# Performance work log

Hardware: AMD Instinct MI355X
Metric: run time of the kernel (lower is better)

## Reference

```python
import jax, jax.numpy as jnp
import numpy as np

N = 50000
E = 1_600_000
IN_C = 128
HID = 128
HEADS = 4
F_OUT = HID // HEADS  # 32
NEG_SLOPE = 0.2


def _glorot(key, shape):
    fan_in, fan_out = shape[0], shape[-1]
    lim = jnp.sqrt(6.0 / (fan_in + fan_out)).astype(jnp.float32)
    return jax.random.uniform(key, shape, jnp.float32, -lim, lim)


def setup_inputs() -> dict:
    key = jax.random.key(0)
    ks = jax.random.split(key, 12)
    x = jax.random.normal(ks[0], (N, IN_C), jnp.float32)
    edge_index = jax.random.randint(ks[1], (2, E), 0, N, jnp.int32)
    # layer 0 params
    W0 = _glorot(ks[2], (IN_C, HEADS * F_OUT))
    att_src0 = _glorot(ks[3], (HEADS, F_OUT))
    att_dst0 = _glorot(ks[4], (HEADS, F_OUT))
    b0 = jnp.zeros((HEADS * F_OUT,), jnp.float32)
    # layer 1 params
    W1 = _glorot(ks[5], (HID, HEADS * F_OUT))
    att_src1 = _glorot(ks[6], (HEADS, F_OUT))
    att_dst1 = _glorot(ks[7], (HEADS, F_OUT))
    b1 = jnp.zeros((HEADS * F_OUT,), jnp.float32)
    return {"x": x, "edge_index": edge_index,
            "W0": W0, "att_src0": att_src0, "att_dst0": att_dst0, "b0": b0,
            "W1": W1, "att_src1": att_src1, "att_dst1": att_dst1, "b1": b1}


def gat_conv(x, src, dst, W, att_src, att_dst, b):
    n = x.shape[0]
    h = (x @ W).reshape(n, HEADS, F_OUT)              # [N,H,F]
    a_s = jnp.einsum('nhf,hf->nh', h, att_src)        # [N,H]
    a_d = jnp.einsum('nhf,hf->nh', h, att_dst)        # [N,H]
    e = jax.nn.leaky_relu(a_s[src] + a_d[dst], NEG_SLOPE)   # [E,H]
    # segment softmax over destination-node neighborhoods
    e_max = jax.ops.segment_max(e, dst, num_segments=n)     # [N,H]
    e_exp = jnp.exp(e - e_max[dst])                          # [E,H]
    denom = jax.ops.segment_sum(e_exp, dst, num_segments=n)  # [N,H]
    denom = jnp.where(denom > 0, denom, 1.0)
    alpha = e_exp / denom[dst]                               # [E,H]
    msg = alpha[:, :, None] * h[src]                         # [E,H,F]
    out = jax.ops.segment_sum(msg, dst, num_segments=n)      # [N,H,F]
    return out.reshape(n, HEADS * F_OUT) + b


def reference(x, edge_index, W0, att_src0, att_dst0, b0, W1, att_src1, att_dst1, b1):
    src, dst = edge_index[0], edge_index[1]
    h = gat_conv(x, src, dst, W0, att_src0, att_dst0, b0)
    h = jax.nn.relu(h)  # dropout p=0.0 / eval mode -> identity
    out = gat_conv(h, src, dst, W1, att_src1, att_dst1, b1)
    return out
```

## Files before the change

### kernel.cpp

```cpp
#include <hip/hip_runtime.h>
#include <hip/hip_fp16.h>

#define N_NODES 50000
#define N_EDGES 1600000
#define NB 196
#define NBLK 256
#define CHUNK (N_EDGES / NBLK)
#define GEMM_BLOCKS 256

typedef _Float16 half8_t __attribute__((ext_vector_type(8)));
typedef _Float16 half2_t __attribute__((ext_vector_type(2)));
typedef float floatx4 __attribute__((ext_vector_type(4)));

#if defined(__has_builtin)
#  if __has_builtin(__builtin_amdgcn_fdot2)
#    define HAS_FDOT2 1
#  endif
#endif
#ifndef HAS_FDOT2
#  define HAS_FDOT2 0
#endif

__global__ __launch_bounds__(256) void gemm_mfma(const float* __restrict__ Xf,
                                                 const __half* __restrict__ Xh,
                                                 int in_half,
                                                 const float* __restrict__ W,
                                                 const float* __restrict__ att_s,
                                                 const float* __restrict__ att_d,
                                                 __half* __restrict__ H16,
                                                 float* __restrict__ as_out,
                                                 float* __restrict__ ad_out, int nrows,
                                                 const int* __restrict__ hist_dst,
                                                 int* __restrict__ hist_totals) {
    __shared__ __align__(16) char lds[49152];
    int t = threadIdx.x;
    if (hist_totals != nullptr && blockIdx.x >= GEMM_BLOCKS) {
        int* hist = reinterpret_cast<int*>(lds);
        int b = blockIdx.x - GEMM_BLOCKS;
        for (int i = t; i < NB; i += 256) hist[i] = 0;
        __syncthreads();
        int s = b * CHUNK;
        for (int i = t; i < CHUNK; i += 256)
            atomicAdd(&hist[hist_dst[s + i] >> 8], 1);
        __syncthreads();
        for (int i = t; i < NB; i += 256)
            if (hist[i]) atomicAdd(&hist_totals[i], hist[i]);
        return;
    }
    char* Alds = lds;
    char* Wlds = lds + 16384;
    int lane = t & 63, wv_ = t >> 6;
    for (int p = 0; p < 16; ++p) {
        int flat = p * 256 + t;
        int k = flat >> 5;
        int n0 = (flat & 31) * 4;
        float4 wv = reinterpret_cast<const float4*>(W)[flat];
        const float* wf = reinterpret_cast<const float*>(&wv);
        #pragma unroll
        for (int i = 0; i < 4; ++i) {
            int n = n0 + i;
            int byte = (n * 256 + k * 2) ^ ((n & 7) << 4);
            *reinterpret_cast<__half*>(Wlds + byte) = __float2half(wf[i]);
        }
    }
    int col16 = lane & 15;
    float Asv[8], Adv[8];
    #pragma unroll
    for (int nt = 0; nt < 8; ++nt) {
        Asv[nt] = att_s[nt * 16 + col16];
        Adv[nt] = att_d[nt * 16 + col16];
    }
    int ksub = (lane >> 4) * 16;
    int rloc = wv_ * 16 + col16;
    int ntiles = (nrows + 63) / 64;
    for (int tile = blockIdx.x; tile < ntiles; tile += GEMM_BLOCKS) {
        int row0 = tile * 64;
        __syncthreads();
        for (int p = 0; p < 8; ++p) {
            int r = p * 8 + (t >> 5);
            int f4 = t & 31;
            int rr = row0 + r;
            uint2 hv = make_uint2(0, 0);
            if (rr < nrows) {
                if (in_half) {
                    hv = *reinterpret_cast<const uint2*>(Xh + (size_t)rr * 128 + f4 * 4);
                } else {
                    float4 xv = reinterpret_cast<const float4*>(Xf)[(size_t)rr * 32 + f4];
                    __half2* hp = reinterpret_cast<__half2*>(&hv);
                    hp[0] = __floats2half2_rn(xv.x, xv.y);
                    hp[1] = __floats2half2_rn(xv.z, xv.w);
                }
            }
            int byte = (r * 256 + f4 * 8) ^ ((r & 7) << 4);
            *reinterpret_cast<uint2*>(Alds + byte) = hv;
        }
        __syncthreads();
        half8_t afr[4];
        #pragma unroll
        for (int kb = 0; kb < 4; ++kb) {
            int byte = (rloc * 256 + kb * 64 + ksub) ^ ((rloc & 7) << 4);
            afr[kb] = *reinterpret_cast<half8_t*>(Alds + byte);
        }
        floatx4 acc[8];
        #pragma unroll
        for (int nt = 0; nt < 8; ++nt) {
            int n = nt * 16 + col16;
            floatx4 a = {0.f, 0.f, 0.f, 0.f};
            #pragma unroll
            for (int kb = 0; kb < 4; ++kb) {
                int byte = (n * 256 + kb * 64 + ksub) ^ ((n & 7) << 4);
                half8_t bfr = *reinterpret_cast<half8_t*>(Wlds + byte);
                a = __builtin_amdgcn_mfma_f32_16x16x32_f16(afr[kb], bfr, a, 0, 0, 0);
            }
            acc[nt] = a;
        }
        float ps[4][4], pd[4][4];
        #pragma unroll
        for (int reg = 0; reg < 4; ++reg)
            #pragma unroll
            for (int h = 0; h < 4; ++h) {
                ps[reg][h] = acc[2*h][reg] * Asv[2*h] + acc[2*h+1][reg] * Asv[2*h+1];
                pd[reg][h] = acc[2*h][reg] * Adv[2*h] + acc[2*h+1][reg] * Adv[2*h+1];
            }
        #pragma unroll
        for (int m = 1; m <= 8; m <<= 1)
            #pragma unroll
            for (int reg = 0; reg < 4; ++reg)
                #pragma unroll
                for (int h = 0; h < 4; ++h) {
                    ps[reg][h] += __shfl_xor(ps[reg][h], m);
                    pd[reg][h] += __shfl_xor(pd[reg][h], m);
                }
        int rbase = row0 + wv_ * 16 + (lane >> 4) * 4;
        #pragma unroll
        for (int reg = 0; reg < 4; ++reg) {
            int grow = rbase + reg;
            if (grow < nrows) {
                #pragma unroll
                for (int nt = 0; nt < 8; ++nt)
                    H16[(size_t)grow * 128 + nt * 16 + col16] = __float2half(acc[nt][reg]);
                if (col16 == 0) {
                    *reinterpret_cast<float4*>(as_out + (size_t)grow * 4) =
                        make_float4(ps[reg][0], ps[reg][1], ps[reg][2], ps[reg][3]);
                    *reinterpret_cast<float4*>(ad_out + (size_t)grow * 4) =
                        make_float4(pd[reg][0], pd[reg][1], pd[reg][2], pd[reg][3]);
                }
            }
        }
    }
}

__global__ __launch_bounds__(1024) void bucket_scatter(const int* __restrict__ src,
                                                       const int* __restrict__ dst,
                                                       const int* __restrict__ btotal,
                                                       int* __restrict__ bcursor,
                                                       int* __restrict__ bucketed) {
    __shared__ int bexcl[NB];
    __shared__ int hist[NB];
    __shared__ int lstart[NB];
    __shared__ int curL[NB];
    __shared__ int gbase[NB];
    __shared__ int recs[CHUNK];
    __shared__ int srt[CHUNK];
    int t = threadIdx.x, b = blockIdx.x;
    int myTot = 0;
    if (t < NB) { myTot = btotal[t]; bexcl[t] = myTot; }
    for (int i = t; i < NB; i += 1024) hist[i] = 0;
    __syncthreads();
    for (int o = 1; o < NB; o <<= 1) {
        int v = (t < NB && t >= o) ? bexcl[t - o] : 0;
        __syncthreads();
        if (t < NB) bexcl[t] += v;
        __syncthreads();
    }
    if (t < NB) bexcl[t] -= myTot;
    int s0 = b * CHUNK;
    for (int i = t; i < CHUNK; i += 1024) {
        unsigned sv = (unsigned)src[s0 + i], dv = (unsigned)dst[s0 + i];
        recs[i] = (int)((sv << 16) | dv);
        atomicAdd(&hist[dv >> 8], 1);
    }
    __syncthreads();
    int myCnt = (t < NB) ? hist[t] : 0;
    if (t < NB) lstart[t] = myCnt;
    __syncthreads();
    for (int o = 1; o < NB; o <<= 1) {
        int v = (t < NB && t >= o) ? lstart[t - o] : 0;
        __syncthreads();
        if (t < NB) lstart[t] += v;
        __syncthreads();
    }
    if (t < NB) {
        int ex = lstart[t] - myCnt;
        lstart[t] = ex;
        curL[t] = ex;
        gbase[t] = bexcl[t] + atomicAdd(&bcursor[t], myCnt);
    }
    __syncthreads();
    for (int i = t; i < CHUNK; i += 1024) {
        int r = recs[i];
        int bk = (int)(((unsigned)r & 0xFFFFu) >> 8);
        int p = atomicAdd(&curL[bk], 1);
        srt[p] = r;
    }
    __syncthreads();
    for (int p = t; p < CHUNK; p += 1024) {
        int r = srt[p];
        unsigned d = (unsigned)r & 0xFFFFu;
        int bk = (int)(d >> 8);
        int g = gbase[bk] + (p - lstart[bk]);
        bucketed[g] = (int)((((unsigned)r >> 16) << 8) | (d & 255u));
    }
}

__global__ __launch_bounds__(1024) void bucket_sort(const int* __restrict__ bucketed,
                                                    const int* __restrict__ btotal,
                                                    int* __restrict__ sorted_packed,
                                                    int* __restrict__ off) {
    __shared__ int bb[NB];
    __shared__ int cnt[256], scn[256], cur[256];
    int t = threadIdx.x, k = blockIdx.x;
    if (t < NB) bb[t] = btotal[t];
    if (t < 256) cnt[t] = 0;
    __syncthreads();
    for (int o = 1; o < NB; o <<= 1) {
        int v = (t < NB && t >= o) ? bb[t - o] : 0;
        __syncthreads();
        if (t < NB) bb[t] += v;
        __syncthreads();
    }
    int base = (k == 0) ? 0 : bb[k - 1];
    int end  = bb[k];
    int m = end - base;
    for (int i = t; i < m; i += 1024)
        atomicAdd(&cnt[bucketed[base + i] & 255], 1);
    __syncthreads();
    if (t < 256) scn[t] = cnt[t];
    __syncthreads();
    for (int o = 1; o < 256; o <<= 1) {
        int v = (t < 256 && t >= o) ? scn[t - o] : 0;
        __syncthreads();
        if (t < 256) scn[t] += v;
        __syncthreads();
    }
    if (t < 256) {
        int excl = scn[t] - cnt[t];
        cur[t] = base + excl;
        int node = k * 256 + t;
        if (node <= N_NODES) off[node] = base + excl;
    }
    __syncthreads();
    for (int i = t; i < m; i += 1024) {
        int rec = bucketed[base + i];
        int p = atomicAdd(&cur[rec & 255], 1);
        sorted_packed[p] = rec;
    }
}

__global__ __launch_bounds__(256) void gat_aggregate_v3(const __half* __restrict__ H16,
                                                        const int* __restrict__ off,
                                                        const int* __restrict__ packed,
                                                        const float* __restrict__ asb,
                                                        const float* __restrict__ adb,
                                                        const float* __restrict__ bias,
                                                        float* __restrict__ OUTF,
                                                        __half* __restrict__ OUTH,
                                                        int n, int mode) {
    int wid = (blockIdx.x * 256 + threadIdx.x) >> 6;
    int lane = threadIdx.x & 63;
    if (wid >= n) return;
    int s = off[wid], e = off[wid + 1];
    int q = lane >> 4;
    int sub = lane & 15;
    int head4 = (sub >> 2) * 4;
    int sub16 = sub * 16;
    float adv = adb[(size_t)wid * 4 + (sub >> 2)];
    const char* Hc = reinterpret_cast<const char*>(H16);
    const char* Ac = reinterpret_cast<const char*>(asb);
    float acc[8] = {0, 0, 0, 0, 0, 0, 0, 0};
    float den = 0.f;
    if (s < e) {
        int idx[4]; float sc[4];
        #pragma unroll
        for (int u = 0; u < 4; ++u) {
            int ii = s + q + u * 4;
            int jj = ii < e ? ii : s;
            idx[u] = packed[jj] & 0xFFFFFF00;
            sc[u] = *reinterpret_cast<const float*>(Ac + (idx[u] >> 4) + head4);
        }
        for (int i = s; i < e; i += 16) {
            uint4 h0 = *reinterpret_cast<const uint4*>(Hc + idx[0] + sub16);
            uint4 h1 = *reinterpret_cast<const uint4*>(Hc + idx[1] + sub16);
            uint4 h2 = *reinterpret_cast<const uint4*>(Hc + idx[2] + sub16);
            uint4 h3 = *reinterpret_cast<const uint4*>(Hc + idx[3] + sub16);
            float w[4];
            #pragma unroll
            for (int u = 0; u < 4; ++u) {
                float ev = sc[u] + adv; ev = fmaxf(ev, 0.2f * ev);
                w[u] = (i + q + u * 4 < e) ? __expf(ev) : 0.f;
            }
            #pragma unroll
            for (int u = 0; u < 4; ++u) {
                int ii = i + 16 + q + u * 4;
                int jj = ii < e ? ii : s;
                idx[u] = packed[jj] & 0xFFFFFF00;
                sc[u] = *reinterpret_cast<const float*>(Ac + (idx[u] >> 4) + head4);
            }
            den += (w[0] + w[1]) + (w[2] + w[3]);
#if HAS_FDOT2
            half2_t w01 = __builtin_bit_cast(half2_t, __builtin_amdgcn_cvt_pkrtz(w[0], w[1]));
            half2_t w23 = __builtin_bit_cast(half2_t, __builtin_amdgcn_cvt_pkrtz(w[2], w[3]));
            const uint* a0 = reinterpret_cast<const uint*>(&h0);
            const uint* a1 = reinterpret_cast<const uint*>(&h1);
            const uint* a2 = reinterpret_cast<const uint*>(&h2);
            const uint* a3 = reinterpret_cast<const uint*>(&h3);
            #pragma unroll
            for (int j = 0; j < 4; ++j) {
                uint p0 = __builtin_amdgcn_perm(a1[j], a0[j], 0x05040100u);
                uint p1 = __builtin_amdgcn_perm(a1[j], a0[j], 0x07060302u);
                uint r0 = __builtin_amdgcn_perm(a3[j], a2[j], 0x05040100u);
                uint r1 = __builtin_amdgcn_perm(a3[j], a2[j], 0x07060302u);
                acc[2*j]   = __builtin_amdgcn_fdot2(__builtin_bit_cast(half2_t, p0), w01,
                             __builtin_amdgcn_fdot2(__builtin_bit_cast(half2_t, r0), w23, acc[2*j],   false), false);
                acc[2*j+1] = __builtin_amdgcn_fdot2(__builtin_bit_cast(half2_t, p1), w01,
                             __builtin_amdgcn_fdot2(__builtin_bit_cast(half2_t, r1), w23, acc[2*j+1], false), false);
            }
#else
            const __half2* pa = reinterpret_cast<const __half2*>(&h0);
            const __half2* pb = reinterpret_cast<const __half2*>(&h1);
            const __half2* pc = reinterpret_cast<const __half2*>(&h2);
            const __half2* pd_ = reinterpret_cast<const __half2*>(&h3);
            #pragma unroll
            for (int j = 0; j < 4; ++j) {
                float2 fa = __half22float2(pa[j]);
                float2 fb = __half22float2(pb[j]);
                float2 fc = __half22float2(pc[j]);
                float2 fd = __half22float2(pd_[j]);
                acc[2*j]   += w[0] * fa.x + w[1] * fb.x + w[2] * fc.x + w[3] * fd.x;
                acc[2*j+1] += w[0] * fa.y + w[1] * fb.y + w[2] * fc.y + w[3] * fd.y;
            }
#endif
        }
    }
    #pragma unroll
    for (int j = 0; j < 8; ++j) acc[j] += __shfl_xor(acc[j], 16);
    den += __shfl_xor(den, 16);
    #pragma unroll
    for (int j = 0; j < 8; ++j) acc[j] += __shfl_xor(acc[j], 32);
    den += __shfl_xor(den, 32);
    if (q == 0) {
        float inv = den > 0.f ? 1.f / den : 0.f;
        float4 b0 = *reinterpret_cast<const float4*>(bias + sub * 8);
        float4 b1 = *reinterpret_cast<const float4*>(bias + sub * 8 + 4);
        float o[8];
        o[0] = acc[0]*inv + b0.x; o[1] = acc[1]*inv + b0.y;
        o[2] = acc[2]*inv + b0.z; o[3] = acc[3]*inv + b0.w;
        o[4] = acc[4]*inv + b1.x; o[5] = acc[5]*inv + b1.y;
        o[6] = acc[6]*inv + b1.z; o[7] = acc[7]*inv + b1.w;
        if (mode) {
            uint4 u;
            __half2* up = reinterpret_cast<__half2*>(&u);
            #pragma unroll
            for (int j = 0; j < 4; ++j)
                up[j] = __floats2half2_rn(fmaxf(o[2*j], 0.f), fmaxf(o[2*j+1], 0.f));
            *reinterpret_cast<uint4*>(OUTH + (size_t)wid * 128 + sub * 8) = u;
        } else {
            *reinterpret_cast<float4*>(OUTF + (size_t)wid * 128 + sub * 8) =
                make_float4(o[0], o[1], o[2], o[3]);
            *reinterpret_cast<float4*>(OUTF + (size_t)wid * 128 + sub * 8 + 4) =
                make_float4(o[4], o[5], o[6], o[7]);
        }
    }
}

extern "C" void kernel_launch(void* const* d_in, const int* in_sizes, int n_in,
                              void* d_out, int out_size, void* d_ws, size_t ws_size,
                              hipStream_t stream) {
    const float* x        = (const float*)d_in[0];
    const int*   edge     = (const int*)d_in[1];
    const float* W0       = (const float*)d_in[2];
    const float* att_src0 = (const float*)d_in[3];
    const float* att_dst0 = (const float*)d_in[4];
    const float* b0       = (const float*)d_in[5];
    const float* W1       = (const float*)d_in[6];
    const float* att_src1 = (const float*)d_in[7];
    const float* att_dst1 = (const float*)d_in[8];
    const float* b1       = (const float*)d_in[9];
    const int* src = edge;
    const int* dst = edge + N_EDGES;
    float* out = (float*)d_out;

    char* ws = (char*)d_ws;
    size_t o = 0;
    auto alloc = [&](size_t bytes) { char* p = ws + o; o += (bytes + 255) & ~(size_t)255; return p; };
    __half* H16   = (__half*)alloc((size_t)N_NODES * 128 * 2);
    float* asb    = (float*)alloc((size_t)N_NODES * 4 * 4);
    float* adb    = (float*)alloc((size_t)N_NODES * 4 * 4);
    int*   off    = (int*)alloc((size_t)(N_NODES + 1) * 4);
    int*   sorted = (int*)alloc((size_t)N_EDGES * 4);
    size_t mark = o;
    int*   btot2    = (int*)alloc((size_t)2 * NB * 4);
    int*   bucketed = (int*)alloc((size_t)N_EDGES * 4);
    __half* h1_16 = (__half*)(ws + mark);
    int* btotal  = btot2;
    int* bcursor = btot2 + NB;

    int agg_blocks = N_NODES / 4;

    hipMemsetAsync(btot2, 0, (size_t)2 * NB * 4, stream);
    gemm_mfma<<<GEMM_BLOCKS + NBLK, 256, 0, stream>>>(x, (const __half*)nullptr, 0,
                                                      W0, att_src0, att_dst0,
                                                      H16, asb, adb, N_NODES, dst, btotal);
    bucket_scatter<<<NBLK, 1024, 0, stream>>>(src, dst, btotal, bcursor, bucketed);
    bucket_sort<<<NB, 1024, 0, stream>>>(bucketed, btotal, sorted, off);

    gat_aggregate_v3<<<agg_blocks, 256, 0, stream>>>(H16, off, sorted, asb, adb, b0,
                                                     (float*)nullptr, h1_16, N_NODES, 1);

    gemm_mfma<<<GEMM_BLOCKS, 256, 0, stream>>>((const float*)nullptr, h1_16, 1,
                                               W1, att_src1, att_dst1,
                                               H16, asb, adb, N_NODES,
                                               (const int*)nullptr, (int*)nullptr);
    gat_aggregate_v3<<<agg_blocks, 256, 0, stream>>>(H16, off, sorted, asb, adb, b1,
                                                     out, (__half*)nullptr, N_NODES, 0);
}
```

Measured before the change: 202.8 us.

## Overlap edge bucket scatter with layer-0 GEMM and use one-wave aggregate blocks

The destination histogram moves into its own small kernel. The bucket-scatter pass is folded into the layer-0 GEMM launch as extra 256-thread blocks, each handling a smaller edge chunk, so scatter work runs concurrently with the MFMA GEMM instead of as a separate serialized launch. The aggregation kernel now launches one 64-thread block per node instead of four waves per block, giving the scheduler finer granularity for load balance across nodes with uneven degree. The cost is an extra kernel launch for the histogram, more blocks for the aggregate, and scatter blocks competing with GEMM blocks for LDS and CUs.

```diff
diff --git a/kernel.cpp b/kernel.cpp
--- a/kernel.cpp
+++ b/kernel.cpp
@@ -4,8 +4,10 @@
 #define N_NODES 50000
 #define N_EDGES 1600000
 #define NB 196
-#define NBLK 256
-#define CHUNK (N_EDGES / NBLK)
+#define NBLK_H 256
+#define CHUNK_H (N_EDGES / NBLK_H)
+#define NBLK_S 512
+#define CHUNK_S (N_EDGES / NBLK_S)
 #define GEMM_BLOCKS 256
 
 typedef _Float16 half8_t __attribute__((ext_vector_type(8)));
@@ -20,6 +22,19 @@
 #ifndef HAS_FDOT2
 #  define HAS_FDOT2 0
 #endif
+
+__global__ __launch_bounds__(256) void edge_hist(const int* __restrict__ dst,
+                                                 int* __restrict__ totals) {
+    __shared__ int hist[NB];
+    int t = threadIdx.x, b = blockIdx.x;
+    if (t < NB) hist[t] = 0;
+    __syncthreads();
+    int s = b * CHUNK_H;
+    for (int i = t; i < CHUNK_H; i += 256)
+        atomicAdd(&hist[dst[s + i] >> 8], 1);
+    __syncthreads();
+    if (t < NB && hist[t]) atomicAdd(&totals[t], hist[t]);
+}
 
 __global__ __launch_bounds__(256) void gemm_mfma(const float* __restrict__ Xf,
                                                  const __half* __restrict__ Xh,
@@ -30,21 +45,70 @@
                                                  __half* __restrict__ H16,
                                                  float* __restrict__ as_out,
                                                  float* __restrict__ ad_out, int nrows,
-                                                 const int* __restrict__ hist_dst,
-                                                 int* __restrict__ hist_totals) {
+                                                 const int* __restrict__ e_src,
+                                                 const int* __restrict__ e_dst,
+                                                 const int* __restrict__ btotal,
+                                                 int* __restrict__ bcursor,
+                                                 int* __restrict__ bucketed,
+                                                 int with_scatter) {
     __shared__ __align__(16) char lds[49152];
     int t = threadIdx.x;
-    if (hist_totals != nullptr && blockIdx.x >= GEMM_BLOCKS) {
-        int* hist = reinterpret_cast<int*>(lds);
+    if (with_scatter && blockIdx.x >= GEMM_BLOCKS) {
+        int* recs   = reinterpret_cast<int*>(lds);
+        int* srt    = reinterpret_cast<int*>(lds + 12800);
+        int* bexcl  = reinterpret_cast<int*>(lds + 25600);
+        int* hist   = reinterpret_cast<int*>(lds + 26624);
+        int* lstart = reinterpret_cast<int*>(lds + 27648);
+        int* curL   = reinterpret_cast<int*>(lds + 28672);
+        int* gbase  = reinterpret_cast<int*>(lds + 29696);
         int b = blockIdx.x - GEMM_BLOCKS;
-        for (int i = t; i < NB; i += 256) hist[i] = 0;
-        __syncthreads();
-        int s = b * CHUNK;
-        for (int i = t; i < CHUNK; i += 256)
-            atomicAdd(&hist[hist_dst[s + i] >> 8], 1);
-        __syncthreads();
-        for (int i = t; i < NB; i += 256)
-            if (hist[i]) atomicAdd(&hist_totals[i], hist[i]);
+        int myTot = 0;
+        if (t < NB) { myTot = btotal[t]; bexcl[t] = myTot; hist[t] = 0; }
+        __syncthreads();
+        for (int o = 1; o < NB; o <<= 1) {
+            int v = (t < NB && t >= o) ? bexcl[t - o] : 0;
+            __syncthreads();
+            if (t < NB) bexcl[t] += v;
+            __syncthreads();
+        }
+        if (t < NB) bexcl[t] -= myTot;
+        int s0 = b * CHUNK_S;
+        for (int i = t; i < CHUNK_S; i += 256) {
+            unsigned sv = (unsigned)e_src[s0 + i], dv = (unsigned)e_dst[s0 + i];
+            recs[i] = (int)((sv << 16) | dv);
+            atomicAdd(&hist[dv >> 8], 1);
+        }
+        __syncthreads();
+        int myCnt = (t < NB) ? hist[t] : 0;
+        if (t < NB) lstart[t] = myCnt;
+        __syncthreads();
+        for (int o = 1; o < NB; o <<= 1) {
+            int v = (t < NB && t >= o) ? lstart[t - o] : 0;
+            __syncthreads();
+            if (t < NB) lstart[t] += v;
+            __syncthreads();
+        }
+        if (t < NB) {
+            int ex = lstart[t] - myCnt;
+            lstart[t] = ex;
+            curL[t] = ex;
+            gbase[t] = bexcl[t] + atomicAdd(&bcursor[t], myCnt);
+        }
+        __syncthreads();
+        for (int i = t; i < CHUNK_S; i += 256) {
+            int r = recs[i];
+            int bk = (int)(((unsigned)r & 0xFFFFu) >> 8);
+            int p = atomicAdd(&curL[bk], 1);
+            srt[p] = r;
+        }
+        __syncthreads();
+        for (int p = t; p < CHUNK_S; p += 256) {
+            int r = srt[p];
+            unsigned d = (unsigned)r & 0xFFFFu;
+            int bk = (int)(d >> 8);
+            int g = gbase[bk] + (p - lstart[bk]);
+            bucketed[g] = (int)((((unsigned)r >> 16) << 8) | (d & 255u));
+        }
         return;
     }
     char* Alds = lds;
@@ -150,69 +214,6 @@
     }
 }
 
-__global__ __launch_bounds__(1024) void bucket_scatter(const int* __restrict__ src,
-                                                       const int* __restrict__ dst,
-                                                       const int* __restrict__ btotal,
-                                                       int* __restrict__ bcursor,
-                                                       int* __restrict__ bucketed) {
-    __shared__ int bexcl[NB];
-    __shared__ int hist[NB];
-    __shared__ int lstart[NB];
-    __shared__ int curL[NB];
-    __shared__ int gbase[NB];
-    __shared__ int recs[CHUNK];
-    __shared__ int srt[CHUNK];
-    int t = threadIdx.x, b = blockIdx.x;
-    int myTot = 0;
-    if (t < NB) { myTot = btotal[t]; bexcl[t] = myTot; }
-    for (int i = t; i < NB; i += 1024) hist[i] = 0;
-    __syncthreads();
-    for (int o = 1; o < NB; o <<= 1) {
-        int v = (t < NB && t >= o) ? bexcl[t - o] : 0;
-        __syncthreads();
-        if (t < NB) bexcl[t] += v;
-        __syncthreads();
-    }
-    if (t < NB) bexcl[t] -= myTot;
-    int s0 = b * CHUNK;
-    for (int i = t; i < CHUNK; i += 1024) {
-        unsigned sv = (unsigned)src[s0 + i], dv = (unsigned)dst[s0 + i];
-        recs[i] = (int)((sv << 16) | dv);
-        atomicAdd(&hist[dv >> 8], 1);
-    }
-    __syncthreads();
-    int myCnt = (t < NB) ? hist[t] : 0;
-    if (t < NB) lstart[t] = myCnt;
-    __syncthreads();
-    for (int o = 1; o < NB; o <<= 1) {
-        int v = (t < NB && t >= o) ? lstart[t - o] : 0;
-        __syncthreads();
-        if (t < NB) lstart[t] += v;
-        __syncthreads();
-    }
-    if (t < NB) {
-        int ex = lstart[t] - myCnt;
-        lstart[t] = ex;
-        curL[t] = ex;
-        gbase[t] = bexcl[t] + atomicAdd(&bcursor[t], myCnt);
-    }
-    __syncthreads();
-    for (int i = t; i < CHUNK; i += 1024) {
-        int r = recs[i];
-        int bk = (int)(((unsigned)r & 0xFFFFu) >> 8);
-        int p = atomicAdd(&curL[bk], 1);
-        srt[p] = r;
-    }
-    __syncthreads();
-    for (int p = t; p < CHUNK; p += 1024) {
-        int r = srt[p];
-        unsigned d = (unsigned)r & 0xFFFFu;
-        int bk = (int)(d >> 8);
-        int g = gbase[bk] + (p - lstart[bk]);
-        bucketed[g] = (int)((((unsigned)r >> 16) << 8) | (d & 255u));
-    }
-}
-
 __global__ __launch_bounds__(1024) void bucket_sort(const int* __restrict__ bucketed,
                                                     const int* __restrict__ btotal,
                                                     int* __restrict__ sorted_packed,
@@ -257,17 +258,17 @@
     }
 }
 
-__global__ __launch_bounds__(256) void gat_aggregate_v3(const __half* __restrict__ H16,
-                                                        const int* __restrict__ off,
-                                                        const int* __restrict__ packed,
-                                                        const float* __restrict__ asb,
-                                                        const float* __restrict__ adb,
-                                                        const float* __restrict__ bias,
-                                                        float* __restrict__ OUTF,
-                                                        __half* __restrict__ OUTH,
-                                                        int n, int mode) {
-    int wid = (blockIdx.x * 256 + threadIdx.x) >> 6;
-    int lane = threadIdx.x & 63;
+__global__ __launch_bounds__(64, 8) void gat_aggregate_v4(const __half* __restrict__ H16,
+                                                          const int* __restrict__ off,
+                                                          const int* __restrict__ packed,
+                                                          const float* __restrict__ asb,
+                                                          const float* __restrict__ adb,
+                                                          const float* __restrict__ bias,
+                                                          float* __restrict__ OUTF,
+                                                          __half* __restrict__ OUTH,
+                                                          int n, int mode) {
+    int wid = blockIdx.x;
+    int lane = threadIdx.x;
     if (wid >= n) return;
     int s = off[wid], e = off[wid + 1];
     int q = lane >> 4;
@@ -401,26 +402,29 @@
     size_t mark = o;
     int*   btot2    = (int*)alloc((size_t)2 * NB * 4);
     int*   bucketed = (int*)alloc((size_t)N_EDGES * 4);
+    (void)alloc((size_t)N_NODES * 128 * 2 > ((size_t)2*NB*4 + (size_t)N_EDGES*4)
+                ? (size_t)N_NODES * 128 * 2 - ((size_t)2*NB*4 + 512 + (size_t)N_EDGES*4) : 0);
     __half* h1_16 = (__half*)(ws + mark);
     int* btotal  = btot2;
     int* bcursor = btot2 + NB;
 
-    int agg_blocks = N_NODES / 4;
-
     hipMemsetAsync(btot2, 0, (size_t)2 * NB * 4, stream);
-    gemm_mfma<<<GEMM_BLOCKS + NBLK, 256, 0, stream>>>(x, (const __half*)nullptr, 0,
-                                                      W0, att_src0, att_dst0,
-                                                      H16, asb, adb, N_NODES, dst, btotal);
-    bucket_scatter<<<NBLK, 1024, 0, stream>>>(src, dst, btotal, bcursor, bucketed);
+    edge_hist<<<NBLK_H, 256, 0, stream>>>(dst, btotal);
+
+    gemm_mfma<<<GEMM_BLOCKS + NBLK_S, 256, 0, stream>>>(x, (const __half*)nullptr, 0,
+                                                        W0, att_src0, att_dst0,
+                                                        H16, asb, adb, N_NODES,
+                                                        src, dst, btotal, bcursor, bucketed, 1);
     bucket_sort<<<NB, 1024, 0, stream>>>(bucketed, btotal, sorted, off);
 
-    gat_aggregate_v3<<<agg_blocks, 256, 0, stream>>>(H16, off, sorted, asb, adb, b0,
-                                                     (float*)nullptr, h1_16, N_NODES, 1);
+    gat_aggregate_v4<<<N_NODES, 64, 0, stream>>>(H16, off, sorted, asb, adb, b0,
+                                                 (float*)nullptr, h1_16, N_NODES, 1);
 
     gemm_mfma<<<GEMM_BLOCKS, 256, 0, stream>>>((const float*)nullptr, h1_16, 1,
                                                W1, att_src1, att_dst1,
                                                H16, asb, adb, N_NODES,
-                                               (const int*)nullptr, (int*)nullptr);
-    gat_aggregate_v3<<<agg_blocks, 256, 0, stream>>>(H16, off, sorted, asb, adb, b1,
-                                                     out, (__half*)nullptr, N_NODES, 0);
+                                               (const int*)nullptr, (const int*)nullptr,
+                                               (const int*)nullptr, (int*)nullptr, (int*)nullptr, 0);
+    gat_aggregate_v4<<<N_NODES, 64, 0, stream>>>(H16, off, sorted, asb, adb, b1,
+                                                 out, (__half*)nullptr, N_NODES, 0);
 }
```

Result: slower. 207.8 us (+2.4%).
